# Kernel tuning notes

Hardware: AMD Instinct MI355X
Metric: run time of the kernel (lower is better)

The kernel has to match this reference:

```python
import jax, jax.numpy as jnp
import numpy as np

N_NODES = 100000
N_EDGES = 625000
D = 128


def setup_inputs() -> dict:
    key = jax.random.key(0)
    ks = jax.random.split(key, 5)
    x = jax.random.normal(ks[0], (N_NODES, D), dtype=jnp.float32)
    edge_index = jax.random.randint(ks[1], (2, N_EDGES), 0, N_NODES, dtype=jnp.int64)
    scale = 1.0 / np.sqrt(D)
    W_neigh = jax.random.normal(ks[2], (D, D), dtype=jnp.float32) * scale
    W_self = jax.random.normal(ks[3], (D, D), dtype=jnp.float32) * scale
    b_self = jax.random.normal(ks[4], (D,), dtype=jnp.float32) * scale
    return {"x": x, "edge_index": edge_index, "W_neigh": W_neigh,
            "W_self": W_self, "b_self": b_self}


def reference(x, edge_index, W_neigh, W_self, b_self):
    src, dst = edge_index[0], edge_index[1]
    n = x.shape[0]
    # mean aggregation over incoming neighbors: segment-sum of x[src] into dst
    neigh = jax.ops.segment_sum(x[src], dst, num_segments=n)  # [N, D]
    counts = jax.ops.segment_sum(jnp.ones((src.shape[0],), dtype=x.dtype), dst,
                                 num_segments=n)  # [N]
    neigh = neigh / jnp.maximum(counts, 1.0)[:, None]
    # lin_self(x) + lin_neigh(neigh); nn.Linear computes x @ W.T + b
    return x @ W_self.T + b_self + neigh @ W_neigh.T
```

## Files before the change

kernel.cpp:

```cpp
#include <hip/hip_runtime.h>
#include <hip/hip_bf16.h>
#include <stdint.h>

#define DFEAT 128
#define CAP 40
#define CURSTRIDE 4

typedef __attribute__((ext_vector_type(8))) short short8;
typedef __attribute__((ext_vector_type(4))) float f32x4;

static __device__ __forceinline__ unsigned short f2bf(float f) {
    union { float f; uint32_t u; } v; v.f = f;
    uint32_t u = v.u;
    u += 0x7FFFu + ((u >> 16) & 1u);
    return (unsigned short)(u >> 16);
}

static __device__ __forceinline__ float lo_bf(uint32_t u) {
    union { uint32_t u; float f; } v; v.u = u << 16; return v.f;
}
static __device__ __forceinline__ float hi_bf(uint32_t u) {
    union { uint32_t u; float f; } v; v.u = u & 0xFFFF0000u; return v.f;
}

static __device__ __forceinline__ short8 pack8(const float4& a, const float4& b) {
    short8 r;
    r[0] = (short)f2bf(a.x); r[1] = (short)f2bf(a.y);
    r[2] = (short)f2bf(a.z); r[3] = (short)f2bf(a.w);
    r[4] = (short)f2bf(b.x); r[5] = (short)f2bf(b.y);
    r[6] = (short)f2bf(b.z); r[7] = (short)f2bf(b.w);
    return r;
}

static __device__ __forceinline__ short8 pack8v(const f32x4& a, const f32x4& b) {
    short8 r;
    r[0] = (short)f2bf(a[0]); r[1] = (short)f2bf(a[1]);
    r[2] = (short)f2bf(a[2]); r[3] = (short)f2bf(a[3]);
    r[4] = (short)f2bf(b[0]); r[5] = (short)f2bf(b[1]);
    r[6] = (short)f2bf(b[2]); r[7] = (short)f2bf(b[3]);
    return r;
}

__global__ __launch_bounds__(256) void sage_prep(
    const float* __restrict__ x, unsigned short* __restrict__ xb, int total8,
    const int* __restrict__ ei, int* __restrict__ cur, int* __restrict__ nbr,
    int E, int EH, int edgeBlocks) {
    int bid = blockIdx.x;
    if (bid < edgeBlocks) {
        int et = bid * 256 + threadIdx.x;
        if (et < EH) {
            int e0 = et;
            int e1 = et + EH;
            bool has1 = e1 < E;
            int s0 = ei[e0];
            int d0 = ei[E + e0];
            int s1 = 0, d1 = 0;
            if (has1) { s1 = ei[e1]; d1 = ei[E + e1]; }
            int slot0 = atomicAdd(&cur[d0 * CURSTRIDE], 1);
            int slot1 = has1 ? atomicAdd(&cur[d1 * CURSTRIDE], 1) : CAP;
            if (slot0 < CAP) nbr[(size_t)d0 * CAP + slot0] = s0;
            if (has1 && slot1 < CAP) nbr[(size_t)d1 * CAP + slot1] = s1;
        }
    } else {
        int i = (bid - edgeBlocks) * 256 + threadIdx.x;
        if (i < total8) {
            const f32x4* xp = (const f32x4*)x;
            f32x4 a = __builtin_nontemporal_load(&xp[2 * i]);
            f32x4 b = __builtin_nontemporal_load(&xp[2 * i + 1]);
            short8 r = pack8v(a, b);
            __builtin_nontemporal_store(r, &((short8*)xb)[i]);
        }
    }
}

__global__ __launch_bounds__(256) void sage_gather(
    const unsigned short* __restrict__ xb, const int* __restrict__ cur,
    const int* __restrict__ nbr, unsigned short* __restrict__ accb, int N) {
    int t = threadIdx.x;
    int wave = t >> 6;
    int lane = t & 63;
    int grp = lane >> 4;
    int sl = lane & 15;
    int node = blockIdx.x * 16 + wave * 4 + grp;
    if (node >= N) return;

    int degTrue = cur[node * CURSTRIDE];
    int deg = degTrue < CAP ? degTrue : CAP;
    const int* nb = nbr + (size_t)node * CAP;

    float acc[8] = {0.f, 0.f, 0.f, 0.f, 0.f, 0.f, 0.f, 0.f};

    for (int j0 = 0; j0 < deg; j0 += 8) {
        int last = deg - 1;
        int idx[8];
        #pragma unroll
        for (int k = 0; k < 8; ++k) {
            int jj = j0 + k;
            idx[k] = nb[jj < deg ? jj : last];
        }
        uint4 u[8];
        #pragma unroll
        for (int k = 0; k < 8; ++k)
            u[k] = ((const uint4*)(xb + (size_t)idx[k] * DFEAT))[sl];
        #pragma unroll
        for (int k = 0; k < 8; ++k) {
            if (j0 + k < deg) {
                acc[0] += lo_bf(u[k].x); acc[1] += hi_bf(u[k].x);
                acc[2] += lo_bf(u[k].y); acc[3] += hi_bf(u[k].y);
                acc[4] += lo_bf(u[k].z); acc[5] += hi_bf(u[k].z);
                acc[6] += lo_bf(u[k].w); acc[7] += hi_bf(u[k].w);
            }
        }
    }

    float inv = 1.0f / fmaxf((float)degTrue, 1.0f);
    uint4 o;
    o.x = (uint32_t)f2bf(acc[0] * inv) | ((uint32_t)f2bf(acc[1] * inv) << 16);
    o.y = (uint32_t)f2bf(acc[2] * inv) | ((uint32_t)f2bf(acc[3] * inv) << 16);
    o.z = (uint32_t)f2bf(acc[4] * inv) | ((uint32_t)f2bf(acc[5] * inv) << 16);
    o.w = (uint32_t)f2bf(acc[6] * inv) | ((uint32_t)f2bf(acc[7] * inv) << 16);
    ((uint4*)(accb + (size_t)node * DFEAT))[sl] = o;
}

__global__ __launch_bounds__(256) void sage_gemm(
    const unsigned short* __restrict__ xb,
    const unsigned short* __restrict__ accb,
    const float* __restrict__ Ws,
    const float* __restrict__ Wn,
    const float* __restrict__ bias,
    float* __restrict__ out,
    int N, int numTiles) {
    __shared__ unsigned short wlds[128 * 256];

    int t = threadIdx.x;
    #pragma unroll
    for (int it = 0; it < 16; ++it) {
        int id = it * 256 + t;
        int n  = id >> 5;
        int c  = id & 31;
        const float* srcw = (c < 16) ? (Ws + n * 128 + c * 8)
                                     : (Wn + n * 128 + (c - 16) * 8);
        int cs = c ^ (n & 7);
        float4 u0 = *(const float4*)(srcw);
        float4 u1 = *(const float4*)(srcw + 4);
        *(short8*)(wlds + n * 256 + cs * 8) = pack8(u0, u1);
    }
    __syncthreads();

    int lane = t & 63;
    int wave = t >> 6;
    int m = lane & 15;
    int q = lane >> 4;

    for (int tile = blockIdx.x; tile < numTiles; tile += gridDim.x) {
        int arow = tile * 64 + wave * 16 + m;
        bool valid = arow < N;

        short8 afrag[8];
        if (valid) {
            const unsigned short* xr = xb   + (size_t)arow * DFEAT;
            const unsigned short* ar = accb + (size_t)arow * DFEAT;
            #pragma unroll
            for (int tt = 0; tt < 4; ++tt) {
                afrag[tt]     = *(const short8*)(xr + tt * 32 + q * 8);
                afrag[4 + tt] = *(const short8*)(ar + tt * 32 + q * 8);
            }
        } else {
            #pragma unroll
            for (int tt = 0; tt < 8; ++tt) {
                short8 z = {0, 0, 0, 0, 0, 0, 0, 0};
                afrag[tt] = z;
            }
        }

        int orow_base = tile * 64 + wave * 16 + q * 4;
        #pragma unroll
        for (int jt = 0; jt < 8; ++jt) {
            f32x4 c4 = {0.f, 0.f, 0.f, 0.f};
            int n = jt * 16 + m;
            #pragma unroll
            for (int tt = 0; tt < 8; ++tt) {
                int c = tt * 4 + q;
                int cs = c ^ (n & 7);
                short8 bfrag = *(const short8*)(wlds + n * 256 + cs * 8);
                c4 = __builtin_amdgcn_mfma_f32_16x16x32_bf16(afrag[tt], bfrag, c4, 0, 0, 0);
            }
            float bv = bias[n];
            #pragma unroll
            for (int r = 0; r < 4; ++r) {
                int orow = orow_base + r;
                if (orow < N)
                    __builtin_nontemporal_store(c4[r] + bv,
                                                &out[(size_t)orow * DFEAT + n]);
            }
        }
    }
}

extern "C" void kernel_launch(void* const* d_in, const int* in_sizes, int n_in,
                              void* d_out, int out_size, void* d_ws, size_t ws_size,
                              hipStream_t stream) {
    const float* x  = (const float*)d_in[0];
    const int*   ei = (const int*)d_in[1];
    const float* Wn = (const float*)d_in[2];
    const float* Ws = (const float*)d_in[3];
    const float* b  = (const float*)d_in[4];
    float* out = (float*)d_out;

    int N = in_sizes[0] / DFEAT;
    int E = in_sizes[1] / 2;

    int* cur = (int*)d_ws;
    int* nbr = cur + (size_t)N * CURSTRIDE;
    unsigned short* xbuf = (unsigned short*)(nbr + (size_t)N * CAP);
    unsigned short* accb = xbuf + (size_t)N * DFEAT;

    hipMemsetAsync(cur, 0, (size_t)N * CURSTRIDE * sizeof(int), stream);

    int total8 = N * DFEAT / 8;
    int EH = (E + 1) / 2;
    int edgeBlocks = (EH + 255) / 256;
    int convBlocks = (total8 + 255) / 256;
    sage_prep<<<edgeBlocks + convBlocks, 256, 0, stream>>>(
        x, xbuf, total8, ei, cur, nbr, E, EH, edgeBlocks);
    sage_gather<<<(N + 15) / 16, 256, 0, stream>>>(xbuf, cur, nbr, accb, N);

    int numTiles = (N + 63) / 64;
    sage_gemm<<<512, 256, 0, stream>>>(xbuf, accb, Ws, Wn, b, out, N, numTiles);
}
```

Before: 197.3 us.

## Fuse bf16 conversion into gather, gather fp32 rows, enlarge GEMM blocks

Result: slower. 333.8 us (+69.1%).

```diff
diff --git a/kernel.cpp b/kernel.cpp
--- a/kernel.cpp
+++ b/kernel.cpp
@@ -16,13 +16,6 @@
     return (unsigned short)(u >> 16);
 }
 
-static __device__ __forceinline__ float lo_bf(uint32_t u) {
-    union { uint32_t u; float f; } v; v.u = u << 16; return v.f;
-}
-static __device__ __forceinline__ float hi_bf(uint32_t u) {
-    union { uint32_t u; float f; } v; v.u = u & 0xFFFF0000u; return v.f;
-}
-
 static __device__ __forceinline__ short8 pack8(const float4& a, const float4& b) {
     short8 r;
     r[0] = (short)f2bf(a.x); r[1] = (short)f2bf(a.y);
@@ -32,63 +25,47 @@
     return r;
 }
 
-static __device__ __forceinline__ short8 pack8v(const f32x4& a, const f32x4& b) {
-    short8 r;
-    r[0] = (short)f2bf(a[0]); r[1] = (short)f2bf(a[1]);
-    r[2] = (short)f2bf(a[2]); r[3] = (short)f2bf(a[3]);
-    r[4] = (short)f2bf(b[0]); r[5] = (short)f2bf(b[1]);
-    r[6] = (short)f2bf(b[2]); r[7] = (short)f2bf(b[3]);
-    return r;
+__global__ __launch_bounds__(256) void sage_fill(
+    const int* __restrict__ ei, int* __restrict__ cur, int* __restrict__ nbr,
+    int E, int EH) {
+    int et = blockIdx.x * 256 + threadIdx.x;
+    if (et >= EH) return;
+    int e0 = et;
+    int e1 = et + EH;
+    bool has1 = e1 < E;
+    int s0 = ei[e0];
+    int d0 = ei[E + e0];
+    int s1 = 0, d1 = 0;
+    if (has1) { s1 = ei[e1]; d1 = ei[E + e1]; }
+    int slot0 = atomicAdd(&cur[d0 * CURSTRIDE], 1);
+    int slot1 = has1 ? atomicAdd(&cur[d1 * CURSTRIDE], 1) : CAP;
+    if (slot0 < CAP) nbr[(size_t)d0 * CAP + slot0] = s0;
+    if (has1 && slot1 < CAP) nbr[(size_t)d1 * CAP + slot1] = s1;
 }
 
-__global__ __launch_bounds__(256) void sage_prep(
-    const float* __restrict__ x, unsigned short* __restrict__ xb, int total8,
-    const int* __restrict__ ei, int* __restrict__ cur, int* __restrict__ nbr,
-    int E, int EH, int edgeBlocks) {
-    int bid = blockIdx.x;
-    if (bid < edgeBlocks) {
-        int et = bid * 256 + threadIdx.x;
-        if (et < EH) {
-            int e0 = et;
-            int e1 = et + EH;
-            bool has1 = e1 < E;
-            int s0 = ei[e0];
-            int d0 = ei[E + e0];
-            int s1 = 0, d1 = 0;
-            if (has1) { s1 = ei[e1]; d1 = ei[E + e1]; }
-            int slot0 = atomicAdd(&cur[d0 * CURSTRIDE], 1);
-            int slot1 = has1 ? atomicAdd(&cur[d1 * CURSTRIDE], 1) : CAP;
-            if (slot0 < CAP) nbr[(size_t)d0 * CAP + slot0] = s0;
-            if (has1 && slot1 < CAP) nbr[(size_t)d1 * CAP + slot1] = s1;
-        }
-    } else {
-        int i = (bid - edgeBlocks) * 256 + threadIdx.x;
-        if (i < total8) {
-            const f32x4* xp = (const f32x4*)x;
-            f32x4 a = __builtin_nontemporal_load(&xp[2 * i]);
-            f32x4 b = __builtin_nontemporal_load(&xp[2 * i + 1]);
-            short8 r = pack8v(a, b);
-            __builtin_nontemporal_store(r, &((short8*)xb)[i]);
-        }
-    }
-}
-
-__global__ __launch_bounds__(256) void sage_gather(
-    const unsigned short* __restrict__ xb, const int* __restrict__ cur,
-    const int* __restrict__ nbr, unsigned short* __restrict__ accb, int N) {
+__global__ __launch_bounds__(256) void sage_gatherconv(
+    const float* __restrict__ x, const int* __restrict__ cur,
+    const int* __restrict__ nbr, unsigned short* __restrict__ xb,
+    unsigned short* __restrict__ accb, int N) {
     int t = threadIdx.x;
     int wave = t >> 6;
     int lane = t & 63;
-    int grp = lane >> 4;
-    int sl = lane & 15;
-    int node = blockIdx.x * 16 + wave * 4 + grp;
+    int grp = lane >> 5;
+    int sl = lane & 31;
+    int node = blockIdx.x * 8 + wave * 2 + grp;
     if (node >= N) return;
+
+    f32x4 self = ((const f32x4*)(x + (size_t)node * DFEAT))[sl];
+    uint2 so;
+    so.x = (uint32_t)f2bf(self[0]) | ((uint32_t)f2bf(self[1]) << 16);
+    so.y = (uint32_t)f2bf(self[2]) | ((uint32_t)f2bf(self[3]) << 16);
+    ((uint2*)(xb + (size_t)node * DFEAT))[sl] = so;
 
     int degTrue = cur[node * CURSTRIDE];
     int deg = degTrue < CAP ? degTrue : CAP;
     const int* nb = nbr + (size_t)node * CAP;
 
-    float acc[8] = {0.f, 0.f, 0.f, 0.f, 0.f, 0.f, 0.f, 0.f};
+    f32x4 acc = {0.f, 0.f, 0.f, 0.f};
 
     for (int j0 = 0; j0 < deg; j0 += 8) {
         int last = deg - 1;
@@ -98,31 +75,27 @@
             int jj = j0 + k;
             idx[k] = nb[jj < deg ? jj : last];
         }
-        uint4 u[8];
+        f32x4 u[8];
         #pragma unroll
         for (int k = 0; k < 8; ++k)
-            u[k] = ((const uint4*)(xb + (size_t)idx[k] * DFEAT))[sl];
+            u[k] = ((const f32x4*)(x + (size_t)idx[k] * DFEAT))[sl];
         #pragma unroll
         for (int k = 0; k < 8; ++k) {
             if (j0 + k < deg) {
-                acc[0] += lo_bf(u[k].x); acc[1] += hi_bf(u[k].x);
-                acc[2] += lo_bf(u[k].y); acc[3] += hi_bf(u[k].y);
-                acc[4] += lo_bf(u[k].z); acc[5] += hi_bf(u[k].z);
-                acc[6] += lo_bf(u[k].w); acc[7] += hi_bf(u[k].w);
+                acc[0] += u[k][0]; acc[1] += u[k][1];
+                acc[2] += u[k][2]; acc[3] += u[k][3];
             }
         }
     }
 
     float inv = 1.0f / fmaxf((float)degTrue, 1.0f);
-    uint4 o;
+    uint2 o;
     o.x = (uint32_t)f2bf(acc[0] * inv) | ((uint32_t)f2bf(acc[1] * inv) << 16);
     o.y = (uint32_t)f2bf(acc[2] * inv) | ((uint32_t)f2bf(acc[3] * inv) << 16);
-    o.z = (uint32_t)f2bf(acc[4] * inv) | ((uint32_t)f2bf(acc[5] * inv) << 16);
-    o.w = (uint32_t)f2bf(acc[6] * inv) | ((uint32_t)f2bf(acc[7] * inv) << 16);
-    ((uint4*)(accb + (size_t)node * DFEAT))[sl] = o;
+    ((uint2*)(accb + (size_t)node * DFEAT))[sl] = o;
 }
 
-__global__ __launch_bounds__(256) void sage_gemm(
+__global__ __launch_bounds__(512, 4) void sage_gemm(
     const unsigned short* __restrict__ xb,
     const unsigned short* __restrict__ accb,
     const float* __restrict__ Ws,
@@ -134,8 +107,8 @@
 
     int t = threadIdx.x;
     #pragma unroll
-    for (int it = 0; it < 16; ++it) {
-        int id = it * 256 + t;
+    for (int it = 0; it < 8; ++it) {
+        int id = it * 512 + t;
         int n  = id >> 5;
         int c  = id & 31;
         const float* srcw = (c < 16) ? (Ws + n * 128 + c * 8)
@@ -153,7 +126,7 @@
     int q = lane >> 4;
 
     for (int tile = blockIdx.x; tile < numTiles; tile += gridDim.x) {
-        int arow = tile * 64 + wave * 16 + m;
+        int arow = tile * 128 + wave * 16 + m;
         bool valid = arow < N;
 
         short8 afrag[8];
@@ -173,7 +146,7 @@
             }
         }
 
-        int orow_base = tile * 64 + wave * 16 + q * 4;
+        int orow_base = tile * 128 + wave * 16 + q * 4;
         #pragma unroll
         for (int jt = 0; jt < 8; ++jt) {
             f32x4 c4 = {0.f, 0.f, 0.f, 0.f};
@@ -217,14 +190,10 @@
 
     hipMemsetAsync(cur, 0, (size_t)N * CURSTRIDE * sizeof(int), stream);
 
-    int total8 = N * DFEAT / 8;
     int EH = (E + 1) / 2;
-    int edgeBlocks = (EH + 255) / 256;
-    int convBlocks = (total8 + 255) / 256;
-    sage_prep<<<edgeBlocks + convBlocks, 256, 0, stream>>>(
-        x, xbuf, total8, ei, cur, nbr, E, EH, edgeBlocks);
-    sage_gather<<<(N + 15) / 16, 256, 0, stream>>>(xbuf, cur, nbr, accb, N);
+    sage_fill<<<(EH + 255) / 256, 256, 0, stream>>>(ei, cur, nbr, E, EH);
+    sage_gatherconv<<<(N + 7) / 8, 256, 0, stream>>>(x, cur, nbr, xbuf, accb, N);
 
-    int numTiles = (N + 63) / 64;
-    sage_gemm<<<512, 256, 0, stream>>>(xbuf, accb, Ws, Wn, b, out, N, numTiles);
+    int numTiles = (N + 127) / 128;
+    sage_gemm<<<512, 512, 0, stream>>>(xbuf, accb, Ws, Wn, b, out, N, numTiles);
 }
```
